# Performance work log

Measured on AMD Instinct MI355X. Metric: run time of the kernel, lower is better.

## Reference

```python
import jax, jax.numpy as jnp
import numpy as np
from jax import lax

DIM = 768
HEADS = 12
EXPERTS = 4
CAPS = [0.4, 0.3, 0.2, 0.1]  # capacity fraction per expert e=0..E-1 (e=E-1 is the full-dim expert)
EPS = 1e-5


def _layernorm(x, g, b):
    mu = jnp.mean(x, axis=-1, keepdims=True)
    var = jnp.mean(jnp.square(x - mu), axis=-1, keepdims=True)
    return (x - mu) * lax.rsqrt(var + EPS) * g + b


def _route(x, router_w, router_b):
    # Expert-preferred capacity router: experts (largest dim first) greedily take
    # their top-capacity tokens by router probability among still-unassigned tokens.
    B, N, _ = x.shape
    probs = jax.nn.softmax(x @ router_w + router_b, axis=-1)  # [B,N,E]
    ks = [int(c * N) for c in CAPS]
    ks[-1] += N - sum(ks)  # remainder to the largest expert
    assigned = jnp.zeros((B, N), dtype=jnp.int32)
    avail = jnp.ones((B, N), dtype=bool)
    brow = jnp.arange(B)[:, None]
    for e in reversed(range(EXPERTS)):
        pe = jnp.where(avail, probs[:, :, e], -jnp.inf)
        _, idx = lax.top_k(pe, ks[e])  # [B, k_e]
        sel = jnp.zeros((B, N), dtype=bool).at[brow, idx].set(True)
        assigned = jnp.where(sel, e, assigned)
        avail = avail & ~sel
    router_probs = jnp.take_along_axis(probs, assigned[..., None], axis=-1)[..., 0]  # [B,N]
    return assigned, router_probs


def _feat_mask(token_mask, dtype):
    # expert e uses the first DIM / 2^(E-1-e) features (nested slicing)
    dims = jnp.array([DIM >> (EXPERTS - 1 - e) for e in range(EXPERTS)], dtype=jnp.int32)
    d_tok = dims[token_mask]  # [B,N]
    return (jnp.arange(DIM)[None, None, :] < d_tok[..., None]).astype(dtype)  # [B,N,D]


def _nested_attention(h, mask, wqkv, bqkv, wo, bo):
    # masking input + output of a full projection == using the top-left nested submatrix
    B, N, D = h.shape
    hd = D // HEADS
    qkv = ((h * mask) @ wqkv + bqkv) * jnp.tile(mask, (1, 1, 3))  # [B,N,3D]
    q, k, v = jnp.split(qkv, 3, axis=-1)
    q = q.reshape(B, N, HEADS, hd).transpose(0, 2, 1, 3)  # [B,H,N,hd]
    k = k.reshape(B, N, HEADS, hd).transpose(0, 2, 1, 3)
    v = v.reshape(B, N, HEADS, hd).transpose(0, 2, 1, 3)
    scores = jnp.einsum('bhqd,bhkd->bhqk', q, k) * (hd ** -0.5)
    attn = jax.nn.softmax(scores, axis=-1)
    out = jnp.einsum('bhqk,bhkd->bhqd', attn, v)  # [B,H,N,hd]
    out = out.transpose(0, 2, 1, 3).reshape(B, N, D) * mask
    return ((out @ wo) + bo) * mask


def setup_inputs() -> dict:
    key = jax.random.key(0)
    ks = jax.random.split(key, 8)
    B, N, D = 4, 1024, DIM
    s = 0.02
    return {
        'x': jax.random.normal(ks[0], (B, N, D), jnp.float32),
        'ln1_g': jnp.ones((D,), jnp.float32),
        'ln1_b': jnp.zeros((D,), jnp.float32),
        'router_w': jax.random.normal(ks[1], (D, EXPERTS), jnp.float32) * s,
        'router_b': jnp.zeros((EXPERTS,), jnp.float32),
        'wqkv': jax.random.normal(ks[2], (D, 3 * D), jnp.float32) * s,
        'bqkv': jnp.zeros((3 * D,), jnp.float32),
        'wo': jax.random.normal(ks[3], (D, D), jnp.float32) * s,
        'bo': jnp.zeros((D,), jnp.float32),
        'ln2_g': jnp.ones((D,), jnp.float32),
        'ln2_b': jnp.zeros((D,), jnp.float32),
        'w1': jax.random.normal(ks[4], (D, 4 * D), jnp.float32) * s,
        'b1': jnp.zeros((4 * D,), jnp.float32),
        'w2': jax.random.normal(ks[5], (4 * D, D), jnp.float32) * s,
        'b2': jnp.zeros((D,), jnp.float32),
    }


def reference(x, ln1_g, ln1_b, router_w, router_b, wqkv, bqkv, wo, bo,
              ln2_g, ln2_b, w1, b1, w2, b2):
    token_mask, router_probs = _route(x, router_w, router_b)
    mask = _feat_mask(token_mask, x.dtype)  # [B,N,D]
    z = x + _nested_attention(_layernorm(x, ln1_g, ln1_b), mask, wqkv, bqkv, wo, bo)
    h2 = _layernorm(z, ln2_g, ln2_b)
    z_prime = jax.nn.gelu(h2 @ w1 + b1, approximate=False) @ w2 + b2
    # probability-weighted token combine
    return z + router_probs[..., None] * z_prime
```

## Files before the change

kernel.cpp:

```cpp
#include <hip/hip_runtime.h>
#include <math.h>

#define DIM 768
#define NTOK 1024
#define BATCH 4
#define HEADS 12
#define TOKENS (BATCH * NTOK)

typedef __bf16 bf16;
typedef __attribute__((ext_vector_type(8))) __bf16 bf16x8;
typedef __attribute__((ext_vector_type(4))) float floatx4;

__global__ void router_kernel(const float* __restrict__ x,
                              const float* __restrict__ rw,
                              const float* __restrict__ rb,
                              float* __restrict__ probs) {
    int t = blockIdx.x;
    int tid = threadIdx.x;
    const float* xr = x + (size_t)t * DIM;
    double acc[4] = {0, 0, 0, 0};
    for (int k = tid; k < DIM; k += 256) {
        double xv = (double)xr[k];
        acc[0] += xv * (double)rw[k * 4 + 0];
        acc[1] += xv * (double)rw[k * 4 + 1];
        acc[2] += xv * (double)rw[k * 4 + 2];
        acc[3] += xv * (double)rw[k * 4 + 3];
    }
    __shared__ double red[256];
    __shared__ double logits[4];
    for (int e = 0; e < 4; ++e) {
        red[tid] = acc[e];
        __syncthreads();
        for (int s = 128; s > 0; s >>= 1) {
            if (tid < s) red[tid] += red[tid + s];
            __syncthreads();
        }
        if (tid == 0) logits[e] = red[0] + (double)rb[e];
        __syncthreads();
    }
    if (tid == 0) {
        double m = logits[0];
        for (int e = 1; e < 4; ++e) m = fmax(m, logits[e]);
        double s = 0.0, p[4];
        for (int e = 0; e < 4; ++e) { p[e] = exp(logits[e] - m); s += p[e]; }
        for (int e = 0; e < 4; ++e) probs[(size_t)t * 4 + e] = (float)(p[e] / s);
    }
}

__global__ __launch_bounds__(1024) void route_kernel(const float* __restrict__ probs,
                                                     int* __restrict__ dtok_g,
                                                     float* __restrict__ rprobs_g) {
    int b = blockIdx.x;
    int tid = threadIdx.x;
    __shared__ float sp[1024];
    const int ks_e[4] = {409, 307, 204, 104};
    const float* pb = probs + (size_t)b * NTOK * 4;
    int avail = 1, assigned = 0;
    for (int e = 3; e >= 1; --e) {
        __syncthreads();
        float pi = avail ? pb[tid * 4 + e] : -INFINITY;
        sp[tid] = pi;
        __syncthreads();
        int cnt = 0;
#pragma unroll 4
        for (int j = 0; j < 1024; ++j) {
            float pj = sp[j];
            cnt += (pj > pi) || (pj == pi && j < tid);
        }
        if (avail && cnt < ks_e[e]) { assigned = e; avail = 0; }
    }
    dtok_g[b * NTOK + tid] = DIM >> (3 - assigned);
    rprobs_g[b * NTOK + tid] = pb[tid * 4 + assigned];
}

__global__ void ln_mask_kernel(const float* __restrict__ x,
                               const float* __restrict__ g,
                               const float* __restrict__ bta,
                               const int* __restrict__ dtok,
                               bf16* __restrict__ out) {
    int t = blockIdx.x;
    int tid = threadIdx.x;
    const float* xr = x + (size_t)t * DIM;
    float s = 0.0f;
    for (int k = tid; k < DIM; k += 256) s += xr[k];
    __shared__ float red[256];
    red[tid] = s;
    __syncthreads();
    for (int st = 128; st > 0; st >>= 1) {
        if (tid < st) red[tid] += red[tid + st];
        __syncthreads();
    }
    float mu = red[0] / DIM;
    __syncthreads();
    float v = 0.0f;
    for (int k = tid; k < DIM; k += 256) { float d = xr[k] - mu; v += d * d; }
    red[tid] = v;
    __syncthreads();
    for (int st = 128; st > 0; st >>= 1) {
        if (tid < st) red[tid] += red[tid + st];
        __syncthreads();
    }
    float rs = rsqrtf(red[0] / DIM + 1e-5f);
    int d = dtok ? dtok[t] : DIM;
    for (int k = tid; k < DIM; k += 256) {
        float val = (xr[k] - mu) * rs * g[k] + bta[k];
        out[(size_t)t * DIM + k] = (bf16)((k < d) ? val : 0.0f);
    }
}

__global__ __launch_bounds__(256) void transpose_bf16_kernel(const float* __restrict__ W,
                                                             bf16* __restrict__ Wt,
                                                             int K, int N) {
    __shared__ float t[32][33];
    int bx = blockIdx.x * 32;
    int by = blockIdx.y * 32;
    int tx = threadIdx.x, ty = threadIdx.y;
#pragma unroll
    for (int i = 0; i < 4; ++i)
        t[ty + i * 8][tx] = W[(size_t)(by + ty + i * 8) * N + bx + tx];
    __syncthreads();
#pragma unroll
    for (int i = 0; i < 4; ++i)
        Wt[(size_t)(bx + ty + i * 8) * K + by + tx] = (bf16)t[tx][ty + i * 8];
}

#define LDT 40
template <int MODE>
__global__ __launch_bounds__(256) void gemm_mfma(const bf16* __restrict__ A,
                                                 const bf16* __restrict__ Bt,
                                                 const float* __restrict__ bias,
                                                 void* __restrict__ Cout,
                                                 int M, int NN, int K, int Kc,
                                                 const int* __restrict__ dtok,
                                                 const float* __restrict__ aux,
                                                 const float* __restrict__ rp) {
    __shared__ bf16 As[2][128 * LDT];
    __shared__ bf16 Bs[2][128 * LDT];
    int n0 = blockIdx.x * 128;
    int m0 = blockIdx.y * 128;
    int kbase = blockIdx.z * Kc;
    int tid = threadIdx.x;
    int wv = tid >> 6;
    int lane = tid & 63;
    int l16 = lane & 15, q4 = lane >> 4;
    int wm = (wv >> 1) * 64, wn = (wv & 1) * 64;
    const bf16* Ap = A + (size_t)m0 * K + kbase;
    const bf16* Bp = Bt + (size_t)n0 * K + kbase;
    floatx4 pa[2], pb[2];
#pragma unroll
    for (int u = 0; u < 2; ++u) {
        int s = tid + u * 256, row = s >> 2, part = s & 3;
        pa[u] = *(const floatx4*)&Ap[(size_t)row * K + part * 8];
        pb[u] = *(const floatx4*)&Bp[(size_t)row * K + part * 8];
    }
#pragma unroll
    for (int u = 0; u < 2; ++u) {
        int s = tid + u * 256, row = s >> 2, part = s & 3;
        *(floatx4*)&As[0][row * LDT + part * 8] = pa[u];
        *(floatx4*)&Bs[0][row * LDT + part * 8] = pb[u];
    }
    __syncthreads();
    floatx4 acc[4][4] = {};
    int kIters = Kc / 32;
    int cur = 0;
    for (int it = 0; it < kIters; ++it) {
        bool notlast = (it + 1 < kIters);
        if (notlast) {
            int ko = (it + 1) * 32;
#pragma unroll
            for (int u = 0; u < 2; ++u) {
                int s = tid + u * 256, row = s >> 2, part = s & 3;
                pa[u] = *(const floatx4*)&Ap[(size_t)row * K + ko + part * 8];
                pb[u] = *(const floatx4*)&Bp[(size_t)row * K + ko + part * 8];
            }
        }
        bf16x8 af[4], bfr[4];
#pragma unroll
        for (int t = 0; t < 4; ++t) {
            af[t] = *(const bf16x8*)&As[cur][(wm + t * 16 + l16) * LDT + q4 * 8];
            bfr[t] = *(const bf16x8*)&Bs[cur][(wn + t * 16 + l16) * LDT + q4 * 8];
        }
#pragma unroll
        for (int i = 0; i < 4; ++i)
#pragma unroll
            for (int j = 0; j < 4; ++j)
                acc[i][j] = __builtin_amdgcn_mfma_f32_16x16x32_bf16(af[i], bfr[j], acc[i][j], 0, 0, 0);
        if (notlast) {
#pragma unroll
            for (int u = 0; u < 2; ++u) {
                int s = tid + u * 256, row = s >> 2, part = s & 3;
                *(floatx4*)&As[cur ^ 1][row * LDT + part * 8] = pa[u];
                *(floatx4*)&Bs[cur ^ 1][row * LDT + part * 8] = pb[u];
            }
            __syncthreads();
            cur ^= 1;
        }
    }
#pragma unroll
    for (int i = 0; i < 4; ++i) {
#pragma unroll
        for (int j = 0; j < 4; ++j) {
            int col = n0 + wn + j * 16 + l16;
#pragma unroll
            for (int r = 0; r < 4; ++r) {
                int row = m0 + wm + i * 16 + q4 * 4 + r;
                if (MODE == 4) {
                    ((float*)Cout)[(size_t)blockIdx.z * M * NN + (size_t)row * NN + col] =
                        acc[i][j][r];
                    continue;
                }
                float c = acc[i][j][r] + bias[col];
                if (MODE == 0) {
                    int jm = col % 768;
                    c = (jm < dtok[row]) ? c : 0.0f;
                    ((bf16*)Cout)[(size_t)row * NN + col] = (bf16)c;
                } else if (MODE == 1) {
                    c = (col < dtok[row]) ? c : 0.0f;
                    c += aux[(size_t)row * NN + col];
                    ((float*)Cout)[(size_t)row * NN + col] = c;
                } else if (MODE == 2) {
                    c = 0.5f * c * (1.0f + erff(c * 0.70710678118654752f));
                    ((bf16*)Cout)[(size_t)row * NN + col] = (bf16)c;
                } else if (MODE == 3) {
                    c = aux[(size_t)row * NN + col] + rp[row] * c;
                    ((float*)Cout)[(size_t)row * NN + col] = c;
                }
            }
        }
    }
}

__global__ __launch_bounds__(256) void ffn2_reduce(const float* __restrict__ part,
                                                   const float* __restrict__ z,
                                                   const float* __restrict__ bias,
                                                   const float* __restrict__ rp,
                                                   float* __restrict__ out) {
    size_t idx = ((size_t)blockIdx.x * 256 + threadIdx.x) * 4;
    int row = (int)(idx / DIM);
    int col = (int)(idx % DIM);
    floatx4 p0 = *(const floatx4*)&part[idx];
    floatx4 p1 = *(const floatx4*)&part[(size_t)TOKENS * DIM + idx];
    floatx4 zz = *(const floatx4*)&z[idx];
    floatx4 bb = *(const floatx4*)&bias[col];
    float r = rp[row];
    floatx4 o = zz + (p0 + p1 + bb) * r;
    *(floatx4*)&out[idx] = o;
}

#define LDH 72
__global__ __launch_bounds__(256) void attn_mfma(const bf16* __restrict__ qkv,
                                                 const int* __restrict__ dtok,
                                                 bf16* __restrict__ attno) {
    int qt = blockIdx.x;
    int h = blockIdx.y;
    int b = blockIdx.z;
    int tid = threadIdx.x;
    int wv = tid >> 6;
    int lane = tid & 63;
    int l16 = lane & 15, q4 = lane >> 4;
    __shared__ bf16 Qs[64 * LDH];
    __shared__ bf16 Ks[64 * LDH];
    __shared__ bf16 Vt[64 * LDH];
    __shared__ bf16 Ps[4][16 * LDH];
    size_t base = (size_t)b * NTOK * 2304;
    for (int s = tid; s < 512; s += 256) {
        int row = s >> 3, part = s & 7;
        *(floatx4*)&Qs[row * LDH + part * 8] =
            *(const floatx4*)&qkv[base + (size_t)(qt * 64 + row) * 2304 + h * 64 + part * 8];
    }
    floatx4 o[4] = {};
    float m_r[4] = {-INFINITY, -INFINITY, -INFINITY, -INFINITY};
    float l_r[4] = {0.0f, 0.0f, 0.0f, 0.0f};
    for (int kt = 0; kt < 16; ++kt) {
        __syncthreads();
        for (int s = tid; s < 512; s += 256) {
            int row = s >> 3, part = s & 7;
            *(floatx4*)&Ks[row * LDH + part * 8] =
                *(const floatx4*)&qkv[base + (size_t)(kt * 64 + row) * 2304 + 768 + h * 64 + part * 8];
            floatx4 vv =
                *(const floatx4*)&qkv[base + (size_t)(kt * 64 + row) * 2304 + 1536 + h * 64 + part * 8];
            const bf16* vp = (const bf16*)&vv;
#pragma unroll
            for (int j = 0; j < 8; ++j) Vt[(part * 8 + j) * LDH + row] = vp[j];
        }
        __syncthreads();
        floatx4 sc[4] = {};
#pragma unroll
        for (int ch = 0; ch < 2; ++ch) {
            bf16x8 aq = *(const bf16x8*)&Qs[(wv * 16 + l16) * LDH + ch * 32 + q4 * 8];
#pragma unroll
            for (int nt = 0; nt < 4; ++nt) {
                bf16x8 bk = *(const bf16x8*)&Ks[(nt * 16 + l16) * LDH + ch * 32 + q4 * 8];
                sc[nt] = __builtin_amdgcn_mfma_f32_16x16x32_bf16(aq, bk, sc[nt], 0, 0, 0);
            }
        }
        float alpha[4], psum[4];
#pragma unroll
        for (int r = 0; r < 4; ++r) {
            float v0 = fmaxf(fmaxf(sc[0][r], sc[1][r]), fmaxf(sc[2][r], sc[3][r])) * 0.125f;
#pragma unroll
            for (int msk = 1; msk < 16; msk <<= 1) v0 = fmaxf(v0, __shfl_xor(v0, msk));
            float mn = fmaxf(m_r[r], v0);
            alpha[r] = __expf(m_r[r] - mn);
            m_r[r] = mn;
            psum[r] = 0.0f;
        }
#pragma unroll
        for (int nt = 0; nt < 4; ++nt)
#pragma unroll
            for (int r = 0; r < 4; ++r) {
                float p = __expf(sc[nt][r] * 0.125f - m_r[r]);
                psum[r] += p;
                Ps[wv][(q4 * 4 + r) * LDH + nt * 16 + l16] = (bf16)p;
            }
#pragma unroll
        for (int r = 0; r < 4; ++r) {
            float s = psum[r];
#pragma unroll
            for (int msk = 1; msk < 16; msk <<= 1) s += __shfl_xor(s, msk);
            l_r[r] = l_r[r] * alpha[r] + s;
        }
#pragma unroll
        for (int dt = 0; dt < 4; ++dt)
#pragma unroll
            for (int r = 0; r < 4; ++r) o[dt][r] *= alpha[r];
        __syncthreads();
#pragma unroll
        for (int ch = 0; ch < 2; ++ch) {
            bf16x8 ap = *(const bf16x8*)&Ps[wv][l16 * LDH + ch * 32 + q4 * 8];
#pragma unroll
            for (int dt = 0; dt < 4; ++dt) {
                bf16x8 bv = *(const bf16x8*)&Vt[(dt * 16 + l16) * LDH + ch * 32 + q4 * 8];
                o[dt] = __builtin_amdgcn_mfma_f32_16x16x32_bf16(ap, bv, o[dt], 0, 0, 0);
            }
        }
    }
#pragma unroll
    for (int r = 0; r < 4; ++r) {
        int tokrow = qt * 64 + wv * 16 + q4 * 4 + r;
        int dt_tok = dtok[b * NTOK + tokrow];
        float inv = 1.0f / l_r[r];
#pragma unroll
        for (int dt = 0; dt < 4; ++dt) {
            int col = h * 64 + dt * 16 + l16;
            float val = (col < dt_tok) ? o[dt][r] * inv : 0.0f;
            attno[((size_t)b * NTOK + tokrow) * DIM + col] = (bf16)val;
        }
    }
}

extern "C" void kernel_launch(void* const* d_in, const int* in_sizes, int n_in,
                              void* d_out, int out_size, void* d_ws, size_t ws_size,
                              hipStream_t stream) {
    const float* x = (const float*)d_in[0];
    const float* ln1g = (const float*)d_in[1];
    const float* ln1b = (const float*)d_in[2];
    const float* rw = (const float*)d_in[3];
    const float* rb = (const float*)d_in[4];
    const float* wqkv = (const float*)d_in[5];
    const float* bqkv = (const float*)d_in[6];
    const float* wo = (const float*)d_in[7];
    const float* bo = (const float*)d_in[8];
    const float* ln2g = (const float*)d_in[9];
    const float* ln2b = (const float*)d_in[10];
    const float* w1 = (const float*)d_in[11];
    const float* b1 = (const float*)d_in[12];
    const float* w2 = (const float*)d_in[13];
    const float* b2 = (const float*)d_in[14];
    float* out = (float*)d_out;

    char* ws = (char*)d_ws;
    size_t off = 0;
    auto alloc = [&](size_t bytes) {
        void* p = ws + off;
        off = (off + bytes + 255) & ~(size_t)255;
        return p;
    };
    bf16* h1m = (bf16*)alloc(sizeof(bf16) * TOKENS * DIM);
    float* probs = (float*)alloc(sizeof(float) * TOKENS * 4);
    float* rprobs = (float*)alloc(sizeof(float) * TOKENS);
    int* dtok = (int*)alloc(sizeof(int) * TOKENS);
    bf16* qkvb = (bf16*)alloc(sizeof(bf16) * TOKENS * 3 * DIM);
    bf16* attno = (bf16*)alloc(sizeof(bf16) * TOKENS * DIM);
    float* z = (float*)alloc(sizeof(float) * TOKENS * DIM);
    bf16* h2 = (bf16*)alloc(sizeof(bf16) * TOKENS * DIM);
    bf16* ffn1 = (bf16*)alloc(sizeof(bf16) * TOKENS * 4 * DIM);
    bf16* wqkvT = (bf16*)alloc(sizeof(bf16) * DIM * 3 * DIM);
    bf16* woT = (bf16*)alloc(sizeof(bf16) * DIM * DIM);
    bf16* w1T = (bf16*)alloc(sizeof(bf16) * DIM * 4 * DIM);
    bf16* w2T = (bf16*)alloc(sizeof(bf16) * 4 * DIM * DIM);
    float* part = (float*)alloc(sizeof(float) * 2 * TOKENS * DIM);

    dim3 tb(32, 8);
    transpose_bf16_kernel<<<dim3(2304 / 32, 768 / 32), tb, 0, stream>>>(wqkv, wqkvT, 768, 2304);
    transpose_bf16_kernel<<<dim3(768 / 32, 768 / 32), tb, 0, stream>>>(wo, woT, 768, 768);
    transpose_bf16_kernel<<<dim3(3072 / 32, 768 / 32), tb, 0, stream>>>(w1, w1T, 768, 3072);
    transpose_bf16_kernel<<<dim3(768 / 32, 3072 / 32), tb, 0, stream>>>(w2, w2T, 3072, 768);

    router_kernel<<<TOKENS, 256, 0, stream>>>(x, rw, rb, probs);
    route_kernel<<<BATCH, 1024, 0, stream>>>(probs, dtok, rprobs);
    ln_mask_kernel<<<TOKENS, 256, 0, stream>>>(x, ln1g, ln1b, dtok, h1m);
    gemm_mfma<0><<<dim3(2304 / 128, 4096 / 128), 256, 0, stream>>>(
        h1m, wqkvT, bqkv, qkvb, TOKENS, 2304, 768, 768, dtok, nullptr, nullptr);
    attn_mfma<<<dim3(16, 12, 4), 256, 0, stream>>>(qkvb, dtok, attno);
    gemm_mfma<1><<<dim3(768 / 128, 4096 / 128), 256, 0, stream>>>(
        attno, woT, bo, z, TOKENS, 768, 768, 768, dtok, x, nullptr);
    ln_mask_kernel<<<TOKENS, 256, 0, stream>>>(z, ln2g, ln2b, nullptr, h2);
    gemm_mfma<2><<<dim3(3072 / 128, 4096 / 128), 256, 0, stream>>>(
        h2, w1T, b1, ffn1, TOKENS, 3072, 768, 768, nullptr, nullptr, nullptr);
    gemm_mfma<4><<<dim3(768 / 128, 4096 / 128, 2), 256, 0, stream>>>(
        ffn1, w2T, nullptr, part, TOKENS, 768, 3072, 1536, nullptr, nullptr, nullptr);
    ffn2_reduce<<<TOKENS * DIM / 1024, 256, 0, stream>>>(part, z, b2, rprobs, out);
}
```

Measured before the change: 456.9 us.

## Split capacity routing into per-expert passes spread across more blocks

The single-block-per-batch routing kernel is replaced by three templated launches, one per expert, each using 16 blocks of 256 threads instead of 4 blocks of 1024. Availability between passes is carried through a global int buffer, and the rank-count loop now reads shared memory as float4 vectors. The goal is to spread the serial O(N^2) rank counting over more compute units and shorten the route stage. The cost is two extra kernel launches, a global round trip for the availability state, and each block reloading the full probability column.

Result: faster. 444.0 us (-2.8%).

```diff
diff --git a/kernel.cpp b/kernel.cpp
--- a/kernel.cpp
+++ b/kernel.cpp
@@ -47,30 +47,43 @@
     }
 }
 
-__global__ __launch_bounds__(1024) void route_kernel(const float* __restrict__ probs,
-                                                     int* __restrict__ dtok_g,
-                                                     float* __restrict__ rprobs_g) {
-    int b = blockIdx.x;
-    int tid = threadIdx.x;
+template <int E, int KCAP, bool FIRST, bool LAST>
+__global__ __launch_bounds__(256) void route_pass(const float* __restrict__ probs,
+                                                  int* __restrict__ avail,
+                                                  int* __restrict__ dtok_g,
+                                                  float* __restrict__ rprobs_g) {
+    int b = blockIdx.y;
+    int i = blockIdx.x * 256 + threadIdx.x;
+    const float* pb = probs + (size_t)b * NTOK * 4;
     __shared__ float sp[1024];
-    const int ks_e[4] = {409, 307, 204, 104};
-    const float* pb = probs + (size_t)b * NTOK * 4;
-    int avail = 1, assigned = 0;
-    for (int e = 3; e >= 1; --e) {
-        __syncthreads();
-        float pi = avail ? pb[tid * 4 + e] : -INFINITY;
-        sp[tid] = pi;
-        __syncthreads();
-        int cnt = 0;
-#pragma unroll 4
-        for (int j = 0; j < 1024; ++j) {
-            float pj = sp[j];
-            cnt += (pj > pi) || (pj == pi && j < tid);
-        }
-        if (avail && cnt < ks_e[e]) { assigned = e; avail = 0; }
-    }
-    dtok_g[b * NTOK + tid] = DIM >> (3 - assigned);
-    rprobs_g[b * NTOK + tid] = pb[tid * 4 + assigned];
+    for (int j = threadIdx.x; j < 1024; j += 256) {
+        bool av = FIRST ? true : (avail[b * NTOK + j] != 0);
+        sp[j] = av ? pb[j * 4 + E] : -INFINITY;
+    }
+    __syncthreads();
+    bool av_i = FIRST ? true : (avail[b * NTOK + i] != 0);
+    float pi = sp[i];
+    int cnt = 0;
+#pragma unroll 8
+    for (int j0 = 0; j0 < 1024; j0 += 4) {
+        floatx4 pj = *(const floatx4*)&sp[j0];
+        cnt += (pj[0] > pi) || (pj[0] == pi && (j0 + 0) < i);
+        cnt += (pj[1] > pi) || (pj[1] == pi && (j0 + 1) < i);
+        cnt += (pj[2] > pi) || (pj[2] == pi && (j0 + 2) < i);
+        cnt += (pj[3] > pi) || (pj[3] == pi && (j0 + 3) < i);
+    }
+    bool sel = av_i && (cnt < KCAP);
+    if (sel) {
+        dtok_g[b * NTOK + i] = DIM >> (3 - E);
+        rprobs_g[b * NTOK + i] = pb[i * 4 + E];
+    } else if (LAST && av_i) {
+        dtok_g[b * NTOK + i] = DIM >> 3;
+        rprobs_g[b * NTOK + i] = pb[i * 4 + 0];
+    }
+    if (!LAST) {
+        if (FIRST) avail[b * NTOK + i] = sel ? 0 : 1;
+        else if (sel) avail[b * NTOK + i] = 0;
+    }
 }
 
 __global__ void ln_mask_kernel(const float* __restrict__ x,
@@ -380,6 +393,7 @@
     float* probs = (float*)alloc(sizeof(float) * TOKENS * 4);
     float* rprobs = (float*)alloc(sizeof(float) * TOKENS);
     int* dtok = (int*)alloc(sizeof(int) * TOKENS);
+    int* avail = (int*)alloc(sizeof(int) * TOKENS);
     bf16* qkvb = (bf16*)alloc(sizeof(bf16) * TOKENS * 3 * DIM);
     bf16* attno = (bf16*)alloc(sizeof(bf16) * TOKENS * DIM);
     float* z = (float*)alloc(sizeof(float) * TOKENS * DIM);
@@ -398,7 +412,9 @@
     transpose_bf16_kernel<<<dim3(768 / 32, 3072 / 32), tb, 0, stream>>>(w2, w2T, 3072, 768);
 
     router_kernel<<<TOKENS, 256, 0, stream>>>(x, rw, rb, probs);
-    route_kernel<<<BATCH, 1024, 0, stream>>>(probs, dtok, rprobs);
+    route_pass<3, 104, true, false><<<dim3(4, BATCH), 256, 0, stream>>>(probs, avail, dtok, rprobs);
+    route_pass<2, 204, false, false><<<dim3(4, BATCH), 256, 0, stream>>>(probs, avail, dtok, rprobs);
+    route_pass<1, 307, false, true><<<dim3(4, BATCH), 256, 0, stream>>>(probs, avail, dtok, rprobs);
     ln_mask_kernel<<<TOKENS, 256, 0, stream>>>(x, ln1g, ln1b, dtok, h1m);
     gemm_mfma<0><<<dim3(2304 / 128, 4096 / 128), 256, 0, stream>>>(
         h1m, wqkvT, bqkv, qkvb, TOKENS, 2304, 768, 768, dtok, nullptr, nullptr);
```
